# Optimization experiments

Hardware: AMD Instinct MI355X
Metric: run time of the kernel (lower is better)

The kernel has to match this reference:

```python
import jax, jax.numpy as jnp
import numpy as np

BN_EPS = 1e-5


def setup_inputs() -> dict:
    key = jax.random.key(0)
    ks = jax.random.split(key, 13)
    B, C, H, W = 8, 256, 96, 32
    D = C // 2  # inter_channels
    s = 0.05
    return {
        "x": jax.random.normal(ks[0], (B, C, H, W), jnp.float32),
        "g_w": jax.random.normal(ks[1], (D, C), jnp.float32) * s,
        "g_b": jax.random.normal(ks[2], (D,), jnp.float32) * s,
        "theta_w": jax.random.normal(ks[3], (D, C), jnp.float32) * s,
        "theta_b": jax.random.normal(ks[4], (D,), jnp.float32) * s,
        "phi_w": jax.random.normal(ks[5], (D, C), jnp.float32) * s,
        "phi_b": jax.random.normal(ks[6], (D,), jnp.float32) * s,
        "w_w": jax.random.normal(ks[7], (C, D), jnp.float32) * s,
        "w_b": jax.random.normal(ks[8], (C,), jnp.float32) * s,
        "bn_gamma": jax.random.normal(ks[9], (C,), jnp.float32),
        "bn_beta": jax.random.normal(ks[10], (C,), jnp.float32) * s,
        "bn_mean": jax.random.normal(ks[11], (C,), jnp.float32) * s,
        "bn_var": jax.random.uniform(ks[12], (C,), jnp.float32),
    }


def reference(x, g_w, g_b, theta_w, theta_b, phi_w, phi_b, w_w, w_b,
              bn_gamma, bn_beta, bn_mean, bn_var):
    B, C, H, W = x.shape
    N = H * W
    xf = x.reshape(B, C, N)  # flatten spatial: (B, C, N)

    # 1x1 conv projections == per-pixel linear maps
    g_x = jnp.einsum('dc,bcn->bnd', g_w, xf) + g_b            # (B, N, D)
    theta_x = jnp.einsum('dc,bcn->bnd', theta_w, xf) + theta_b  # (B, N, D)
    phi_x = jnp.einsum('dc,bcn->bdn', phi_w, xf) + phi_b[:, None]  # (B, D, N)

    # unnormalized attention: f = theta phi^T / N, then y = f g
    f_div_C = jnp.einsum('bnd,bdm->bnm', theta_x, phi_x) / N  # (B, N, N)
    y = jnp.einsum('bnm,bmd->bnd', f_div_C, g_x)              # (B, N, D)

    # output 1x1 conv + eval-mode BatchNorm2d
    wy = jnp.einsum('cd,bnd->bcn', w_w, y) + w_b[:, None]     # (B, C, N)
    inv = bn_gamma / jnp.sqrt(bn_var + BN_EPS)
    wy = (wy - bn_mean[:, None]) * inv[:, None] + bn_beta[:, None]

    z = wy.reshape(B, C, H, W) + x  # residual
    return z
```

## Files before the change

### kernel.cpp

```cpp
#include <hip/hip_runtime.h>
#include <hip/hip_bf16.h>
#include <cstddef>

typedef __attribute__((ext_vector_type(8))) short short8;
typedef __attribute__((ext_vector_type(4))) float floatx4;
typedef __hip_bfloat16 bf16;

#define NB 8
#define NC 256
#define ND 128
#define NN 3072
#define NBLK 48
#define BN_EPS 1e-5f

static __device__ __forceinline__ short f2s(float v) {
    bf16 h = __float2bfloat16(v);
    return *reinterpret_cast<short*>(&h);
}

__global__ __launch_bounds__(256) void setup_kernel(
    const float* __restrict__ phi_w, const float* __restrict__ g_w,
    const float* __restrict__ theta_w, short* __restrict__ Wall)
{
    int t = threadIdx.x;
    int r = blockIdx.x;
    const float* src = (r < 128) ? (phi_w + (size_t)r * NC)
                     : (r < 256) ? (g_w + (size_t)(r - 128) * NC)
                                 : (theta_w + (size_t)(r - 256) * NC);
    Wall[(size_t)r * NC + t] = f2s(src[t]);
}

__global__ __launch_bounds__(384)
void proj_kernel(const float* __restrict__ x, const short* __restrict__ Wall,
                 const float* __restrict__ phi_b, const float* __restrict__ g_b,
                 const float* __restrict__ theta_b,
                 short* __restrict__ thDN, float* __restrict__ Mpart)
{
    __shared__ short PGs[256][72];
    __shared__ short Xs[64][72];
    int b = blockIdx.y;
    int n0 = blockIdx.x * 64;
    int t = threadIdx.x;
    int lane = t & 63;
    int wave = t >> 6;
    int lm = lane & 15;
    int lk = (lane >> 4) * 8;

    const float* xb = x + (size_t)b * NC * NN;

    floatx4 zero = {0.f, 0.f, 0.f, 0.f};
    floatx4 acc[4][4];
#pragma unroll
    for (int i = 0; i < 4; ++i)
#pragma unroll
        for (int j = 0; j < 4; ++j) acc[i][j] = zero;

#pragma unroll
    for (int kt = 0; kt < NC; kt += 64) {
        __syncthreads();
        if (t < 256) {
            int sn = t & 63, cg = t >> 6;
            const float* src = xb + (size_t)(kt + cg * 16) * NN + n0 + sn;
            short8 s0, s1;
#pragma unroll
            for (int j = 0; j < 8; ++j) {
                s0[j] = f2s(src[(size_t)j * NN]);
                s1[j] = f2s(src[(size_t)(8 + j) * NN]);
            }
            *(short8*)&Xs[sn][cg * 16]     = s0;
            *(short8*)&Xs[sn][cg * 16 + 8] = s1;
        }
        __syncthreads();
#pragma unroll
        for (int kk = 0; kk < 64; kk += 32) {
            short8 af[4], bfr[4];
#pragma unroll
            for (int i = 0; i < 4; ++i)
                af[i] = *(const short8*)(Wall +
                        (size_t)(wave * 64 + i * 16 + lm) * NC + kt + kk + lk);
#pragma unroll
            for (int j = 0; j < 4; ++j)
                bfr[j] = *(const short8*)&Xs[j * 16 + lm][kk + lk];
#pragma unroll
            for (int i = 0; i < 4; ++i)
#pragma unroll
                for (int j = 0; j < 4; ++j)
                    acc[i][j] = __builtin_amdgcn_mfma_f32_16x16x32_bf16(
                        af[i], bfr[j], acc[i][j], 0, 0, 0);
        }
    }

    int row0 = wave * 64 + (lane >> 4) * 4;

    if (wave < 4) {
#pragma unroll
        for (int i = 0; i < 4; ++i) {
#pragma unroll
            for (int r = 0; r < 4; ++r) {
                int row = row0 + i * 16 + r;
                float bv = (row < 128) ? phi_b[row] : g_b[row - 128];
#pragma unroll
                for (int j = 0; j < 4; ++j)
                    PGs[row][lm + j * 16] = f2s(acc[i][j][r] + bv);
            }
        }
    } else {
        short* Tb = thDN + (size_t)b * ND * NN;
#pragma unroll
        for (int i = 0; i < 4; ++i) {
#pragma unroll
            for (int r = 0; r < 4; ++r) {
                int d = row0 - 256 + i * 16 + r;
                float bv = theta_b[d];
#pragma unroll
                for (int j = 0; j < 4; ++j)
                    Tb[(size_t)d * NN + n0 + lm + j * 16] =
                        f2s(acc[i][j][r] + bv);
            }
        }
    }
    __syncthreads();

    if (wave < 4) {
        int wr = wave >> 1, wc = wave & 1;
        floatx4 macc[4][4];
#pragma unroll
        for (int i = 0; i < 4; ++i)
#pragma unroll
            for (int j = 0; j < 4; ++j) macc[i][j] = zero;
#pragma unroll
        for (int kk = 0; kk < 64; kk += 32) {
            short8 af[4], bfr[4];
#pragma unroll
            for (int i = 0; i < 4; ++i)
                af[i] = *(const short8*)&PGs[wr * 64 + i * 16 + lm][kk + lk];
#pragma unroll
            for (int j = 0; j < 4; ++j)
                bfr[j] = *(const short8*)&PGs[128 + wc * 64 + j * 16 + lm][kk + lk];
#pragma unroll
            for (int i = 0; i < 4; ++i)
#pragma unroll
                for (int j = 0; j < 4; ++j)
                    macc[i][j] = __builtin_amdgcn_mfma_f32_16x16x32_bf16(
                        af[i], bfr[j], macc[i][j], 0, 0, 0);
        }
        float* Mf = Mpart + ((size_t)b * NBLK + blockIdx.x) * (ND * ND);
        int mr0 = wr * 64 + (lane >> 4) * 4;
        int mc0 = wc * 64 + lm;
        const float sc = 1.f / (float)NN;
#pragma unroll
        for (int i = 0; i < 4; ++i)
#pragma unroll
            for (int j = 0; j < 4; ++j)
#pragma unroll
                for (int r = 0; r < 4; ++r)
                    Mf[(size_t)(mr0 + i * 16 + r) * ND + mc0 + j * 16] =
                        macc[i][j][r] * sc;
    }
}

__global__ __launch_bounds__(256)
void reduce_kernel(const float* __restrict__ Mpart, short* __restrict__ Mb16)
{
    int idx = blockIdx.x * 256 + threadIdx.x;
    int b = idx >> 14;
    int e = idx & 16383;
    const float* src = Mpart + (size_t)b * NBLK * 16384 + e;
    float s = 0.f;
#pragma unroll 8
    for (int p = 0; p < NBLK; ++p) s += src[(size_t)p * 16384];
    Mb16[(size_t)b * 16384 + e] = f2s(s);
}

__global__ __launch_bounds__(256)
void final_kernel(const short* __restrict__ Mb16, const short* __restrict__ thDN,
                  const float* __restrict__ w_w, const float* __restrict__ w_b,
                  const float* __restrict__ gamma, const float* __restrict__ beta,
                  const float* __restrict__ mean, const float* __restrict__ var,
                  const float* __restrict__ x, float* __restrict__ out)
{
    __shared__ short As[128][72];
    __shared__ short Bs[128][72];
    __shared__ short P2s[128][136];
    int b = blockIdx.z;
    int tile_m = blockIdx.y * 128;
    int tile_n = blockIdx.x * 128;
    int t = threadIdx.x;
    int lane = t & 63;
    int wave = t >> 6;
    int wr = wave >> 1, wc = wave & 1;
    int lm = lane & 15;
    int lk = (lane >> 4) * 8;
    int ch = (t & 7) * 8;
    int r0 = t >> 3;

    const short* Mb = Mb16 + (size_t)b * ND * ND;

    floatx4 zero = {0.f, 0.f, 0.f, 0.f};
    floatx4 acc[4][4];
#pragma unroll
    for (int i = 0; i < 4; ++i)
#pragma unroll
        for (int j = 0; j < 4; ++j) acc[i][j] = zero;

#pragma unroll
    for (int kt = 0; kt < ND; kt += 64) {
        __syncthreads();
#pragma unroll
        for (int p = 0; p < 4; ++p) {
            int r = r0 + p * 32;
            const float* ap = w_w + (size_t)(tile_m + r) * ND + kt + ch;
            floatx4 a0 = *(const floatx4*)ap, a1 = *(const floatx4*)(ap + 4);
            short8 sa;
#pragma unroll
            for (int j = 0; j < 4; ++j) { sa[j] = f2s(a0[j]); sa[4 + j] = f2s(a1[j]); }
            *(short8*)&As[r][ch] = sa;
            *(short8*)&Bs[r][ch] = *(const short8*)(Mb + (size_t)r * ND + kt + ch);
        }
        __syncthreads();
#pragma unroll
        for (int kk = 0; kk < 64; kk += 32) {
            short8 af[4], bfr[4];
#pragma unroll
            for (int i = 0; i < 4; ++i)
                af[i] = *(const short8*)&As[wr * 64 + i * 16 + lm][kk + lk];
#pragma unroll
            for (int j = 0; j < 4; ++j)
                bfr[j] = *(const short8*)&Bs[wc * 64 + j * 16 + lm][kk + lk];
#pragma unroll
            for (int i = 0; i < 4; ++i)
#pragma unroll
                for (int j = 0; j < 4; ++j)
                    acc[i][j] = __builtin_amdgcn_mfma_f32_16x16x32_bf16(
                        af[i], bfr[j], acc[i][j], 0, 0, 0);
        }
    }

    {
        int row0 = wr * 64 + (lane >> 4) * 4;
        int col0 = wc * 64 + lm;
#pragma unroll
        for (int i = 0; i < 4; ++i) {
#pragma unroll
            for (int r = 0; r < 4; ++r) {
                int cl = row0 + i * 16 + r;
                int c = tile_m + cl;
                float iv = gamma[c] * rsqrtf(var[c] + BN_EPS);
#pragma unroll
                for (int j = 0; j < 4; ++j)
                    P2s[cl][col0 + j * 16] = f2s(acc[i][j][r] * iv);
            }
        }
    }

    floatx4 acc2[4][4];
#pragma unroll
    for (int i = 0; i < 4; ++i)
#pragma unroll
        for (int j = 0; j < 4; ++j) acc2[i][j] = zero;

    const short* Tb = thDN + (size_t)b * ND * NN;
#pragma unroll
    for (int kt = 0; kt < ND; kt += 64) {
        __syncthreads();
        {
            int dl = t & 63;
            int ng = t >> 6;
            const short* src = Tb + (size_t)(kt + dl) * NN + tile_n + ng * 32;
#pragma unroll
            for (int q = 0; q < 4; ++q) {
                short8 v = *(const short8*)(src + q * 8);
#pragma unroll
                for (int jj = 0; jj < 8; ++jj)
                    Bs[ng * 32 + q * 8 + jj][dl] = v[jj];
            }
        }
        __syncthreads();
#pragma unroll
        for (int kk = 0; kk < 64; kk += 32) {
            short8 af[4], bfr[4];
#pragma unroll
            for (int i = 0; i < 4; ++i)
                af[i] = *(const short8*)&P2s[wr * 64 + i * 16 + lm][kt + kk + lk];
#pragma unroll
            for (int j = 0; j < 4; ++j)
                bfr[j] = *(const short8*)&Bs[wc * 64 + j * 16 + lm][kk + lk];
#pragma unroll
            for (int i = 0; i < 4; ++i)
#pragma unroll
                for (int j = 0; j < 4; ++j)
                    acc2[i][j] = __builtin_amdgcn_mfma_f32_16x16x32_bf16(
                        af[i], bfr[j], acc2[i][j], 0, 0, 0);
        }
    }

    int crow0 = tile_m + wr * 64 + (lane >> 4) * 4;
    int col0 = tile_n + wc * 64 + lm;
    float* Cf = out + (size_t)b * NC * NN;
    const float* Rg = x + (size_t)b * NC * NN;
#pragma unroll
    for (int i = 0; i < 4; ++i) {
#pragma unroll
        for (int r = 0; r < 4; ++r) {
            int c = crow0 + i * 16 + r;
            float iv = gamma[c] * rsqrtf(var[c] + BN_EPS);
            float b2 = iv * (w_b[c] - mean[c]) + beta[c];
#pragma unroll
            for (int j = 0; j < 4; ++j) {
                size_t idx = (size_t)c * NN + col0 + j * 16;
                Cf[idx] = acc2[i][j][r] + b2 + Rg[idx];
            }
        }
    }
}

extern "C" void kernel_launch(void* const* d_in, const int* in_sizes, int n_in,
                              void* d_out, int out_size, void* d_ws, size_t ws_size,
                              hipStream_t stream)
{
    const float* x       = (const float*)d_in[0];
    const float* g_w     = (const float*)d_in[1];
    const float* g_b     = (const float*)d_in[2];
    const float* theta_w = (const float*)d_in[3];
    const float* theta_b = (const float*)d_in[4];
    const float* phi_w   = (const float*)d_in[5];
    const float* phi_b   = (const float*)d_in[6];
    const float* w_w     = (const float*)d_in[7];
    const float* w_b     = (const float*)d_in[8];
    const float* gamma   = (const float*)d_in[9];
    const float* beta    = (const float*)d_in[10];
    const float* mean    = (const float*)d_in[11];
    const float* var     = (const float*)d_in[12];
    (void)in_sizes; (void)n_in; (void)out_size; (void)ws_size;

    char* w = (char*)d_ws;
    short* thDN  = (short*)w; w += (size_t)NB * ND * NN * 2;
    float* Mpart = (float*)w; w += (size_t)NB * NBLK * ND * ND * 4;
    short* Mb16  = (short*)w; w += (size_t)NB * ND * ND * 2;
    short* Wall  = (short*)w; w += (size_t)384 * NC * 2;

    setup_kernel<<<dim3(384), dim3(256), 0, stream>>>(
        phi_w, g_w, theta_w, Wall);

    proj_kernel<<<dim3(NN / 64, NB), dim3(384), 0, stream>>>(
        x, Wall, phi_b, g_b, theta_b, thDN, Mpart);

    reduce_kernel<<<dim3(512), dim3(256), 0, stream>>>(Mpart, Mb16);

    final_kernel<<<dim3(NN / 128, NC / 128, NB), 256, 0, stream>>>(
        Mb16, thDN, w_w, w_b, gamma, beta, mean, var, x, (float*)d_out);
}
```

Baseline: 135.8 us.

## Store per-block partial products in bf16 fragment layout and prefetch x tiles

The projection kernel now register-prefetches the next x tile from global memory while running MFMAs on the current tile. Per-block partial phi·g^T results are stored as bf16 in the raw MFMA fragment order, so each lane writes coalesced and the partial buffer is half its previous size. The reduce kernel reads 8 bf16 values per thread with vector loads, sums them in fp32 and scatters the result back to row-major layout. It launches far fewer blocks than before. The cost is that partials are rounded to bf16 before the 48-way sum, and the low block count may underfill the GPU.

```diff
diff --git a/kernel.cpp b/kernel.cpp
--- a/kernel.cpp
+++ b/kernel.cpp
@@ -17,6 +17,10 @@
     bf16 h = __float2bfloat16(v);
     return *reinterpret_cast<short*>(&h);
 }
+static __device__ __forceinline__ float s2f(short v) {
+    bf16 h = *reinterpret_cast<bf16*>(&v);
+    return __bfloat162float(h);
+}
 
 __global__ __launch_bounds__(256) void setup_kernel(
     const float* __restrict__ phi_w, const float* __restrict__ g_w,
@@ -34,7 +38,7 @@
 void proj_kernel(const float* __restrict__ x, const short* __restrict__ Wall,
                  const float* __restrict__ phi_b, const float* __restrict__ g_b,
                  const float* __restrict__ theta_b,
-                 short* __restrict__ thDN, float* __restrict__ Mpart)
+                 short* __restrict__ thDN, short* __restrict__ Mpart)
 {
     __shared__ short PGs[256][72];
     __shared__ short Xs[64][72];
@@ -45,6 +49,8 @@
     int wave = t >> 6;
     int lm = lane & 15;
     int lk = (lane >> 4) * 8;
+    int sn = t & 63;
+    int cg = t >> 6;
 
     const float* xb = x + (size_t)b * NC * NN;
 
@@ -55,39 +61,55 @@
 #pragma unroll
         for (int j = 0; j < 4; ++j) acc[i][j] = zero;
 
+    float v[16];
+    if (t < 256) {
+        const float* src = xb + (size_t)(cg * 16) * NN + n0 + sn;
+#pragma unroll
+        for (int j = 0; j < 16; ++j) v[j] = src[(size_t)j * NN];
+    }
+
 #pragma unroll
     for (int kt = 0; kt < NC; kt += 64) {
         __syncthreads();
         if (t < 256) {
-            int sn = t & 63, cg = t >> 6;
-            const float* src = xb + (size_t)(kt + cg * 16) * NN + n0 + sn;
             short8 s0, s1;
 #pragma unroll
-            for (int j = 0; j < 8; ++j) {
-                s0[j] = f2s(src[(size_t)j * NN]);
-                s1[j] = f2s(src[(size_t)(8 + j) * NN]);
-            }
+            for (int j = 0; j < 8; ++j) { s0[j] = f2s(v[j]); s1[j] = f2s(v[8 + j]); }
             *(short8*)&Xs[sn][cg * 16]     = s0;
             *(short8*)&Xs[sn][cg * 16 + 8] = s1;
         }
         __syncthreads();
-#pragma unroll
-        for (int kk = 0; kk < 64; kk += 32) {
-            short8 af[4], bfr[4];
-#pragma unroll
-            for (int i = 0; i < 4; ++i)
-                af[i] = *(const short8*)(Wall +
-                        (size_t)(wave * 64 + i * 16 + lm) * NC + kt + kk + lk);
-#pragma unroll
-            for (int j = 0; j < 4; ++j)
-                bfr[j] = *(const short8*)&Xs[j * 16 + lm][kk + lk];
-#pragma unroll
-            for (int i = 0; i < 4; ++i)
-#pragma unroll
-                for (int j = 0; j < 4; ++j)
-                    acc[i][j] = __builtin_amdgcn_mfma_f32_16x16x32_bf16(
-                        af[i], bfr[j], acc[i][j], 0, 0, 0);
-        }
+        if (t < 256 && kt + 64 < NC) {
+            const float* src = xb + (size_t)(kt + 64 + cg * 16) * NN + n0 + sn;
+#pragma unroll
+            for (int j = 0; j < 16; ++j) v[j] = src[(size_t)j * NN];
+        }
+        short8 a0[4], a1[4];
+#pragma unroll
+        for (int i = 0; i < 4; ++i) {
+            const short* wp = Wall + (size_t)(wave * 64 + i * 16 + lm) * NC + kt + lk;
+            a0[i] = *(const short8*)(wp);
+            a1[i] = *(const short8*)(wp + 32);
+        }
+        short8 bfr[4];
+#pragma unroll
+        for (int j = 0; j < 4; ++j)
+            bfr[j] = *(const short8*)&Xs[j * 16 + lm][lk];
+#pragma unroll
+        for (int i = 0; i < 4; ++i)
+#pragma unroll
+            for (int j = 0; j < 4; ++j)
+                acc[i][j] = __builtin_amdgcn_mfma_f32_16x16x32_bf16(
+                    a0[i], bfr[j], acc[i][j], 0, 0, 0);
+#pragma unroll
+        for (int j = 0; j < 4; ++j)
+            bfr[j] = *(const short8*)&Xs[j * 16 + lm][32 + lk];
+#pragma unroll
+        for (int i = 0; i < 4; ++i)
+#pragma unroll
+            for (int j = 0; j < 4; ++j)
+                acc[i][j] = __builtin_amdgcn_mfma_f32_16x16x32_bf16(
+                    a1[i], bfr[j], acc[i][j], 0, 0, 0);
     }
 
     int row0 = wave * 64 + (lane >> 4) * 4;
@@ -122,54 +144,68 @@
     __syncthreads();
 
     if (wave < 4) {
+        floatx4 macc[4][4];
+#pragma unroll
+        for (int i = 0; i < 4; ++i)
+#pragma unroll
+            for (int j = 0; j < 4; ++j) macc[i][j] = zero;
         int wr = wave >> 1, wc = wave & 1;
-        floatx4 macc[4][4];
+#pragma unroll
+        for (int kk = 0; kk < 64; kk += 32) {
+            short8 af[4], bg[4];
+#pragma unroll
+            for (int i = 0; i < 4; ++i)
+                af[i] = *(const short8*)&PGs[wr * 64 + i * 16 + lm][kk + lk];
+#pragma unroll
+            for (int j = 0; j < 4; ++j)
+                bg[j] = *(const short8*)&PGs[128 + wc * 64 + j * 16 + lm][kk + lk];
+#pragma unroll
+            for (int i = 0; i < 4; ++i)
+#pragma unroll
+                for (int j = 0; j < 4; ++j)
+                    macc[i][j] = __builtin_amdgcn_mfma_f32_16x16x32_bf16(
+                        af[i], bg[j], macc[i][j], 0, 0, 0);
+        }
+        short* Mf = Mpart + ((size_t)b * NBLK + blockIdx.x) * 16384
+                  + (size_t)wave * 4096 + lane;
+        const float sc = 1.f / (float)NN;
 #pragma unroll
         for (int i = 0; i < 4; ++i)
 #pragma unroll
-            for (int j = 0; j < 4; ++j) macc[i][j] = zero;
-#pragma unroll
-        for (int kk = 0; kk < 64; kk += 32) {
-            short8 af[4], bfr[4];
-#pragma unroll
-            for (int i = 0; i < 4; ++i)
-                af[i] = *(const short8*)&PGs[wr * 64 + i * 16 + lm][kk + lk];
-#pragma unroll
-            for (int j = 0; j < 4; ++j)
-                bfr[j] = *(const short8*)&PGs[128 + wc * 64 + j * 16 + lm][kk + lk];
-#pragma unroll
-            for (int i = 0; i < 4; ++i)
-#pragma unroll
-                for (int j = 0; j < 4; ++j)
-                    macc[i][j] = __builtin_amdgcn_mfma_f32_16x16x32_bf16(
-                        af[i], bfr[j], macc[i][j], 0, 0, 0);
-        }
-        float* Mf = Mpart + ((size_t)b * NBLK + blockIdx.x) * (ND * ND);
-        int mr0 = wr * 64 + (lane >> 4) * 4;
-        int mc0 = wc * 64 + lm;
-        const float sc = 1.f / (float)NN;
-#pragma unroll
-        for (int i = 0; i < 4; ++i)
-#pragma unroll
             for (int j = 0; j < 4; ++j)
 #pragma unroll
                 for (int r = 0; r < 4; ++r)
-                    Mf[(size_t)(mr0 + i * 16 + r) * ND + mc0 + j * 16] =
-                        macc[i][j][r] * sc;
+                    Mf[(((i * 4 + j) * 4) + r) * 64] = f2s(macc[i][j][r] * sc);
     }
 }
 
 __global__ __launch_bounds__(256)
-void reduce_kernel(const float* __restrict__ Mpart, short* __restrict__ Mb16)
-{
-    int idx = blockIdx.x * 256 + threadIdx.x;
-    int b = idx >> 14;
-    int e = idx & 16383;
-    const float* src = Mpart + (size_t)b * NBLK * 16384 + e;
-    float s = 0.f;
-#pragma unroll 8
-    for (int p = 0; p < NBLK; ++p) s += src[(size_t)p * 16384];
-    Mb16[(size_t)b * 16384 + e] = f2s(s);
+void reduce_kernel(const short* __restrict__ Mpart, short* __restrict__ Mb16)
+{
+    int tid = blockIdx.x * 256 + threadIdx.x;
+    int b = tid >> 11;
+    int idx = (tid & 2047) * 8;
+    int wave2 = idx >> 12;
+    int rem = idx & 4095;
+    int ijr = rem >> 6;
+    int lane0 = rem & 63;
+    int i = ijr >> 4, j = (ijr >> 2) & 3, r = ijr & 3;
+    int wr = wave2 >> 1, wc = wave2 & 1;
+    int e = wr * 64 + (lane0 >> 4) * 4 + i * 16 + r;
+    int d0 = wc * 64 + (lane0 & 15) + j * 16;
+
+    const short* src = Mpart + (size_t)b * NBLK * 16384 + idx;
+    float s[8] = {0.f, 0.f, 0.f, 0.f, 0.f, 0.f, 0.f, 0.f};
+#pragma unroll 6
+    for (int p = 0; p < NBLK; ++p) {
+        short8 vv = *(const short8*)(src + (size_t)p * 16384);
+#pragma unroll
+        for (int k = 0; k < 8; ++k) s[k] += s2f(vv[k]);
+    }
+    short8 o;
+#pragma unroll
+    for (int k = 0; k < 8; ++k) o[k] = f2s(s[k]);
+    *(short8*)(Mb16 + (size_t)b * 16384 + (size_t)e * ND + d0) = o;
 }
 
 __global__ __launch_bounds__(256)
@@ -269,10 +305,10 @@
             const short* src = Tb + (size_t)(kt + dl) * NN + tile_n + ng * 32;
 #pragma unroll
             for (int q = 0; q < 4; ++q) {
-                short8 v = *(const short8*)(src + q * 8);
+                short8 vv = *(const short8*)(src + q * 8);
 #pragma unroll
                 for (int jj = 0; jj < 8; ++jj)
-                    Bs[ng * 32 + q * 8 + jj][dl] = v[jj];
+                    Bs[ng * 32 + q * 8 + jj][dl] = vv[jj];
             }
         }
         __syncthreads();
@@ -335,7 +371,7 @@
 
     char* w = (char*)d_ws;
     short* thDN  = (short*)w; w += (size_t)NB * ND * NN * 2;
-    float* Mpart = (float*)w; w += (size_t)NB * NBLK * ND * ND * 4;
+    short* Mpart = (short*)w; w += (size_t)NB * NBLK * ND * ND * 2;
     short* Mb16  = (short*)w; w += (size_t)NB * ND * ND * 2;
     short* Wall  = (short*)w; w += (size_t)384 * NC * 2;
 
@@ -345,7 +381,7 @@
     proj_kernel<<<dim3(NN / 64, NB), dim3(384), 0, stream>>>(
         x, Wall, phi_b, g_b, theta_b, thDN, Mpart);
 
-    reduce_kernel<<<dim3(512), dim3(256), 0, stream>>>(Mpart, Mb16);
+    reduce_kernel<<<dim3(64), dim3(256), 0, stream>>>(Mpart, Mb16);
 
     final_kernel<<<dim3(NN / 128, NC / 128, NB), 256, 0, stream>>>(
         Mb16, thDN, w_w, w_b, gamma, beta, mean, var, x, (float*)d_out);
```

Result: no change. 136.9 us (+0.9%).
